# Optimization experiments

Hardware: AMD Instinct MI355X
Metric: run time of the kernel (lower is better)

Reference implementation:

```python
import jax, jax.numpy as jnp
import numpy as np
from jax import lax

B, N, CIN, H, W = 1, 6, 256, 32, 88
COUT = 80
IMG_H, IMG_W = 256, 704
XB = (-51.2, 51.2, 0.8); YB = (-51.2, 51.2, 0.8); ZB = (-5.0, 3.0, 0.8)
NX, NY, NZ = 128, 128, 10
EPS = 1e-5


def _voxel_coords(b0, b1, vs):
    n = int(round((b1 - b0) / vs))
    return jnp.linspace(b0 + 0.5 * vs, b1 - 0.5 * vs, n, dtype=jnp.float32)


def _make_points():
    xs = _voxel_coords(*XB); ys = _voxel_coords(*YB); zs = _voxel_coords(*ZB)
    gx, gy, gz = jnp.meshgrid(xs, ys, zs, indexing='ij')
    return jnp.stack([gx, gy, gz], -1).reshape(-1, 3)  # [M,3], M = NX*NY*NZ


def _conv(x, w, b=None, pad=1):
    y = lax.conv_general_dilated(x, w, (1, 1), [(pad, pad), (pad, pad)],
                                 dimension_numbers=('NCHW', 'OIHW', 'NCHW'))
    if b is not None:
        y = y + b[None, :, None, None]
    return y


def _bn(x, g, b, m, v):
    return (g[None, :, None, None] * (x - m[None, :, None, None])
            * lax.rsqrt(v[None, :, None, None] + EPS) + b[None, :, None, None])


def _bilinear(feat, gx, gy):
    # feat [C,Hf,Wf]; gx,gy [M] in [-1,1]; align_corners=True, zero padding
    C, Hf, Wf = feat.shape
    ix = (gx + 1.0) * 0.5 * (Wf - 1)
    iy = (gy + 1.0) * 0.5 * (Hf - 1)
    ix0 = jnp.floor(ix); iy0 = jnp.floor(iy)
    wx1 = ix - ix0; wy1 = iy - iy0

    def tap(iyf, ixf, wgt):
        valid = (ixf >= 0) & (ixf < Wf) & (iyf >= 0) & (iyf < Hf)
        ii = jnp.clip(ixf, 0, Wf - 1).astype(jnp.int32)
        jj = jnp.clip(iyf, 0, Hf - 1).astype(jnp.int32)
        return feat[:, jj, ii] * (wgt * valid)[None, :]

    return (tap(iy0, ix0, (1 - wy1) * (1 - wx1))
            + tap(iy0, ix0 + 1, (1 - wy1) * wx1)
            + tap(iy0 + 1, ix0, wy1 * (1 - wx1))
            + tap(iy0 + 1, ix0 + 1, wy1 * wx1))


def reference(img, lidar2image, w1, b1, g1, beta1, m1, v1,
              w2, b2, g2, beta2, m2, v2, w3, b3):
    # proj_net: conv3x3+BN+ReLU, conv3x3+BN+ReLU, conv1x1
    x = img.reshape(B * N, CIN, H, W)
    x = jax.nn.relu(_bn(_conv(x, w1, b1), g1, beta1, m1, v1))
    x = jax.nn.relu(_bn(_conv(x, w2, b2), g2, beta2, m2, v2))
    feat = _conv(x, w3, b3, pad=0)  # [B*N, COUT, H, W]

    pts = _make_points()  # [M,3]
    R = lidar2image[:, :, :3, :3].reshape(B * N, 3, 3)
    t = lidar2image[:, :, :3, 3].reshape(B * N, 3, 1)
    proj = jnp.einsum('kij,mj->kim', R, pts) + t  # [BN,3,M]
    dist = proj[:, 2]
    px = proj[:, 0] / dist
    py = proj[:, 1] / dist
    gx = px / IMG_W * 2.0 - 1.0
    gy = py / IMG_H * 2.0 - 1.0

    sampled = jax.vmap(_bilinear)(feat, gx, gy)  # [BN, COUT, M]
    on_img = (px < IMG_W) & (px > 0) & (py < IMG_H) & (py > 0) & (dist > 0.1)
    sampled = jnp.where(on_img[:, None, :], sampled, 0.0)

    vox = sampled.reshape(B, N, COUT, NX, NY, NZ)
    bev = jnp.max(vox, axis=1).mean(axis=-1)  # [B, COUT, NX, NY]
    return bev


def setup_inputs() -> dict:
    key = jax.random.key(0)
    ks = jax.random.split(key, 8)
    img = jax.random.normal(ks[0], (B, N, CIN, H, W), jnp.float32)

    # Plausible lidar->image matrices: 6 cameras in a ring, pinhole intrinsics.
    fx = fy = 280.0; cx = IMG_W / 2.0; cy = IMG_H / 2.0
    K = np.array([[fx, 0.0, cx], [0.0, fy, cy], [0.0, 0.0, 1.0]])
    mats = []
    for k in range(N):
        th = 2.0 * np.pi * k / N
        fwd = np.array([np.cos(th), np.sin(th), 0.0])
        rgt = np.array([np.sin(th), -np.cos(th), 0.0])
        dwn = np.array([0.0, 0.0, -1.0])
        Rm = np.stack([rgt, dwn, fwd], 0)
        c = np.array([0.5 * np.cos(th), 0.5 * np.sin(th), 1.5])
        M4 = np.eye(4)
        M4[:3, :3] = K @ Rm
        M4[:3, 3] = K @ (-Rm @ c)
        mats.append(M4)
    lidar2image = jnp.asarray(np.broadcast_to(np.stack(mats), (B, N, 4, 4)).copy(),
                              jnp.float32)

    def w(k, shape, s=0.02):
        return jax.random.normal(k, shape, jnp.float32) * s

    zc = lambda c: jnp.zeros((c,), jnp.float32)
    oc = lambda c: jnp.ones((c,), jnp.float32)
    return dict(
        img=img, lidar2image=lidar2image,
        w1=w(ks[1], (CIN, CIN, 3, 3)), b1=zc(CIN),
        g1=oc(CIN), beta1=zc(CIN), m1=zc(CIN), v1=oc(CIN),
        w2=w(ks[2], (CIN, CIN, 3, 3)), b2=zc(CIN),
        g2=oc(CIN), beta2=zc(CIN), m2=zc(CIN), v2=oc(CIN),
        w3=w(ks[3], (COUT, CIN, 1, 1)), b3=zc(COUT),
    )
```

## Files before the change

### kernel.cpp

```cpp
#include <hip/hip_runtime.h>
#include <math.h>

#define N_IMG 6
#define CIN   256
#define H_IN  32
#define W_IN  88
#define SP    2816
#define HH    34
#define WW    90
#define SPH   3060
#define COUTC 80
#define EPSBN 1e-5f

typedef _Float16 half8 __attribute__((ext_vector_type(8)));
typedef _Float16 half2v __attribute__((ext_vector_type(2)));
typedef float floatx4 __attribute__((ext_vector_type(4)));

#define AS1 __attribute__((address_space(1)))
#define AS3 __attribute__((address_space(3)))

__global__ __launch_bounds__(256) void zero_halo(_Float16* __restrict__ a,
                                                 _Float16* __restrict__ b) {
  const int im = blockIdx.x;
  const int tid = threadIdx.x;
  for (int s = tid; s < 244 * 32; s += 256) {
    const int pos = s >> 5;
    const int gr  = s & 31;
    int h, w;
    if (pos < 90)       { h = 0;  w = pos; }
    else if (pos < 180) { h = 33; w = pos - 90; }
    else { const int r = pos - 180; h = 1 + (r >> 1); w = (r & 1) * 89; }
    const size_t off = ((size_t)im * SPH + h * WW + w) * CIN + gr * 8;
    half8 z = {};
    *(half8*)(a + off) = z;
    *(half8*)(b + off) = z;
  }
}

__global__ __launch_bounds__(256) void prep_w33(const float* __restrict__ wa,
                                                const float* __restrict__ wb,
                                                _Float16* __restrict__ wTa,
                                                _Float16* __restrict__ wTb) {
  __shared__ float s[2304];
  const int oc = blockIdx.x;
  const int tid = threadIdx.x;
  const float* w = blockIdx.y ? wb : wa;
  _Float16* wT = blockIdx.y ? wTb : wTa;
  const float* wo = w + (size_t)oc * 2304;
  for (int i = tid; i < 2304; i += 256) s[i] = wo[i];
  __syncthreads();
  for (int i = tid; i < 2304; i += 256) {
    const int tap = i >> 8;
    const int ic  = i & 255;
    wT[((size_t)tap * 256 + oc) * 256 + ic] = (_Float16)s[ic * 9 + tap];
  }
}

__global__ __launch_bounds__(256) void prep_w11(const float* __restrict__ w,
                                                _Float16* __restrict__ wT) {
  int idx = blockIdx.x * 256 + threadIdx.x;
  if (idx >= CIN * COUTC) return;
  wT[idx] = (_Float16)w[idx];
}

__global__ __launch_bounds__(256) void nchw_to_nhwc(const float* __restrict__ img,
                                                    _Float16* __restrict__ x0) {
  __shared__ float t[64][65];
  const int sp0 = blockIdx.x * 64;
  const int ic0 = blockIdx.y * 64;
  const int im  = blockIdx.z;
  const int tx = threadIdx.x & 63;
  const int ty = threadIdx.x >> 6;
  for (int r = ty; r < 64; r += 4)
    t[r][tx] = img[((size_t)(im * CIN + ic0 + r)) * SP + sp0 + tx];
  __syncthreads();
  for (int r = ty; r < 64; r += 4) {
    const int sp = sp0 + r;
    const int h = sp / 88;
    const int w = sp - h * 88;
    x0[((size_t)im * SPH + h * WW + w + WW + 1) * CIN + ic0 + tx] = (_Float16)t[tx][r];
  }
}

__global__ __launch_bounds__(256) void conv3x3_mfma(
    const _Float16* __restrict__ x, const _Float16* __restrict__ wT,
    const float* __restrict__ bias, const float* __restrict__ gamma,
    const float* __restrict__ beta, const float* __restrict__ bnm,
    const float* __restrict__ bnv, _Float16* __restrict__ out,
    int OW, int OB, int imStride)
{
  __shared__ _Float16 As[128 * 64];
  __shared__ _Float16 Bs[128 * 64];

  const int tid  = threadIdx.x;
  const int wv   = tid >> 6;
  const int lane = tid & 63;
  const int m0   = blockIdx.x * 128;
  const int n0   = blockIdx.y * 128;
  const int im   = blockIdx.z;
  const _Float16* xim = x + (size_t)im * SPH * CIN;

  int srcA[4], srcB[4];
  #pragma unroll
  for (int i = 0; i < 4; ++i) {
    const int g = i * 256 + wv * 64 + lane;
    const int row = g >> 3;
    const int lg  = (g & 7) ^ (row & 7);
    const int m = m0 + row;
    const int h = m / 88;
    const int w = m - h * 88;
    srcA[i] = ((h + 1) * WW + (w + 1)) * CIN + lg * 8;
    srcB[i] = (n0 + row) * 256 + lg * 8;
  }

  const int fr = lane & 15;
  const int q  = lane >> 4;
  const int q4 = q * 4;
  const int mw = (wv & 1) * 64;
  const int nw = (wv >> 1) * 64;

  floatx4 acc[4][4];
  #pragma unroll
  for (int i = 0; i < 4; ++i)
    #pragma unroll
    for (int j = 0; j < 4; ++j) {
      acc[i][j][0] = 0.f; acc[i][j][1] = 0.f; acc[i][j][2] = 0.f; acc[i][j][3] = 0.f;
    }

  for (int tap = 0; tap < 9; ++tap) {
    const int dy = tap / 3 - 1;
    const int dx = tap - (tap / 3) * 3 - 1;
    const int aoff = (dy * WW + dx) * CIN;
    const size_t boff = (size_t)tap * 65536;

    for (int icc = 0; icc < 256; icc += 64) {
      #pragma unroll
      for (int i = 0; i < 4; ++i)
        __builtin_amdgcn_global_load_lds(
            (const AS1 void*)(xim + srcA[i] + aoff + icc),
            (AS3 void*)(&As[(i * 256 + wv * 64) * 8]), 16, 0, 0);
      #pragma unroll
      for (int i = 0; i < 4; ++i)
        __builtin_amdgcn_global_load_lds(
            (const AS1 void*)(wT + boff + srcB[i] + icc),
            (AS3 void*)(&Bs[(i * 256 + wv * 64) * 8]), 16, 0, 0);
      __syncthreads();

      #pragma unroll
      for (int ks = 0; ks < 2; ++ks) {
        half8 af[4], bf[4];
        #pragma unroll
        for (int i = 0; i < 4; ++i) {
          const int row = mw + i * 16 + fr;
          af[i] = *(const half8*)(&As[row * 64 + (((ks * 4 + q) ^ (row & 7)) * 8)]);
        }
        #pragma unroll
        for (int j = 0; j < 4; ++j) {
          const int row = nw + j * 16 + fr;
          bf[j] = *(const half8*)(&Bs[row * 64 + (((ks * 4 + q) ^ (row & 7)) * 8)]);
        }
        #pragma unroll
        for (int i = 0; i < 4; ++i)
          #pragma unroll
          for (int j = 0; j < 4; ++j)
            acc[i][j] = __builtin_amdgcn_mfma_f32_16x16x32_f16(af[i], bf[j], acc[i][j], 0, 0, 0);
      }
      __syncthreads();
    }
  }

  #pragma unroll
  for (int j = 0; j < 4; ++j) {
    const int oc = n0 + nw + j * 16 + fr;
    const float sc = gamma[oc] * rsqrtf(bnv[oc] + EPSBN);
    const float sh = (bias[oc] - bnm[oc]) * sc + beta[oc];
    #pragma unroll
    for (int i = 0; i < 4; ++i) {
      #pragma unroll
      for (int r = 0; r < 4; ++r) {
        const int m = m0 + mw + i * 16 + q4 + r;
        const int h = m / 88;
        const int w = m - h * 88;
        const float v = fmaxf(fmaf(acc[i][j][r], sc, sh), 0.f);
        out[((size_t)im * imStride + h * OW + w + OB) * CIN + oc] = (_Float16)v;
      }
    }
  }
}

__global__ __launch_bounds__(128) void conv1x1_mfma(
    const _Float16* __restrict__ x, const _Float16* __restrict__ wT,
    const float* __restrict__ bias, _Float16* __restrict__ feat)
{
  __shared__ _Float16 Bs[80 * 264];

  const int tid = threadIdx.x;
  const int m0  = blockIdx.x * 64;
  const int wv   = tid >> 6;
  const int lane = tid & 63;
  const int fr  = lane & 15;
  const int q8  = (lane >> 4) * 8;
  const int q4  = (lane >> 4) * 4;

  for (int g = tid; g < 2560; g += 128) {
    const int oc = g >> 5;
    const int kg8 = (g & 31) << 3;
    *(half8*)(&Bs[oc * 264 + kg8]) = *(const half8*)(wT + oc * 256 + kg8);
  }
  __syncthreads();

  floatx4 acc[2][5];
  #pragma unroll
  for (int i = 0; i < 2; ++i)
    #pragma unroll
    for (int j = 0; j < 5; ++j) {
      acc[i][j][0] = 0.f; acc[i][j][1] = 0.f; acc[i][j][2] = 0.f; acc[i][j][3] = 0.f;
    }

  const _Float16* xa = x + (size_t)(m0 + wv * 32 + fr) * 256 + q8;
  #pragma unroll
  for (int ks = 0; ks < 8; ++ks) {
    half8 af[2], bf[5];
    #pragma unroll
    for (int i = 0; i < 2; ++i)
      af[i] = *(const half8*)(xa + (size_t)i * 16 * 256 + ks * 32);
    #pragma unroll
    for (int j = 0; j < 5; ++j)
      bf[j] = *(const half8*)(&Bs[(j * 16 + fr) * 264 + ks * 32 + q8]);
    #pragma unroll
    for (int i = 0; i < 2; ++i)
      #pragma unroll
      for (int j = 0; j < 5; ++j)
        acc[i][j] = __builtin_amdgcn_mfma_f32_16x16x32_f16(af[i], bf[j], acc[i][j], 0, 0, 0);
  }

  #pragma unroll
  for (int j = 0; j < 5; ++j) {
    const int oc = j * 16 + fr;
    const float bb = bias[oc];
    #pragma unroll
    for (int i = 0; i < 2; ++i) {
      const int mbase = m0 + wv * 32 + i * 16 + q4;
      #pragma unroll
      for (int r = 0; r < 4; ++r)
        feat[(size_t)(mbase + r) * COUTC + oc] = (_Float16)(acc[i][j][r] + bb);
    }
  }
}

__global__ __launch_bounds__(320) void bev_sample(
    const _Float16* __restrict__ feat, const float* __restrict__ l2i,
    float* __restrict__ tmp)
{
  __shared__ int4   eo[480];
  __shared__ float4 ew[480];
  const int tid = threadIdx.x;
  const int cellBase = blockIdx.x * 8;

  for (int e = tid; e < 480; e += 320) {
    const int cell = e / 60;
    const int idx = e - cell * 60;
    const int n = idx / 10;
    const int z = idx - n * 10;
    const int cid = cellBase + cell;
    const int gix = cid >> 7;
    const int giy = cid & 127;
    const float X = (float)(-50.8 + (double)gix * (101.6 / 127.0));
    const float Y = (float)(-50.8 + (double)giy * (101.6 / 127.0));
    const float Z = (float)(-4.6 + (double)z * (7.2 / 9.0));
    const float* M = l2i + n * 16;
    const float pw = M[0] * X + M[1] * Y + M[2] * Z + M[3];
    const float ph = M[4] * X + M[5] * Y + M[6] * Z + M[7];
    const float d  = M[8] * X + M[9] * Y + M[10] * Z + M[11];
    const float px = pw / d;
    const float py = ph / d;
    const bool on_img = (px < 704.f) && (px > 0.f) && (py < 256.f) && (py > 0.f) && (d > 0.1f);
    const float gx = px / 704.f * 2.f - 1.f;
    const float gy = py / 256.f * 2.f - 1.f;
    const float ixf = (gx + 1.f) * 0.5f * 87.f;
    const float iyf = (gy + 1.f) * 0.5f * 31.f;
    const float ix0 = floorf(ixf);
    const float iy0 = floorf(iyf);
    const float wx1 = ixf - ix0;
    const float wy1 = iyf - iy0;
    const float ix1 = ix0 + 1.f, iy1 = iy0 + 1.f;
    float w00 = (1.f - wy1) * (1.f - wx1);
    float w01 = (1.f - wy1) * wx1;
    float w10 = wy1 * (1.f - wx1);
    float w11 = wy1 * wx1;
    const bool vx0 = (ix0 >= 0.f) && (ix0 < 88.f);
    const bool vx1 = (ix1 >= 0.f) && (ix1 < 88.f);
    const bool vy0 = (iy0 >= 0.f) && (iy0 < 32.f);
    const bool vy1 = (iy1 >= 0.f) && (iy1 < 32.f);
    if (!(on_img && vy0 && vx0)) w00 = 0.f;
    if (!(on_img && vy0 && vx1)) w01 = 0.f;
    if (!(on_img && vy1 && vx0)) w10 = 0.f;
    if (!(on_img && vy1 && vx1)) w11 = 0.f;
    const int i0 = (int)fminf(fmaxf(ix0, 0.f), 87.f);
    const int i1 = (int)fminf(fmaxf(ix1, 0.f), 87.f);
    const int j0 = (int)fminf(fmaxf(iy0, 0.f), 31.f);
    const int j1 = (int)fminf(fmaxf(iy1, 0.f), 31.f);
    const int base = n * SP;
    eo[e] = make_int4((base + j0 * 88 + i0) * COUTC,
                      (base + j0 * 88 + i1) * COUTC,
                      (base + j1 * 88 + i0) * COUTC,
                      (base + j1 * 88 + i1) * COUTC);
    ew[e] = make_float4(w00, w01, w10, w11);
  }
  __syncthreads();

  const int c2 = (tid % 40) * 2;
  const int cell = tid / 40;
  const int ebase = cell * 60;
  float a0 = 0.f, a1 = 0.f;
  for (int z = 0; z < 10; ++z) {
    float mx0 = -INFINITY, mx1 = -INFINITY;
    #pragma unroll
    for (int n = 0; n < 6; ++n) {
      const float4 w = ew[ebase + n * 10 + z];
      if (w.x + w.y + w.z + w.w > 0.f) {
        const int4 o = eo[ebase + n * 10 + z];
        const half2v p00 = *(const half2v*)(feat + o.x + c2);
        const half2v p01 = *(const half2v*)(feat + o.y + c2);
        const half2v p10 = *(const half2v*)(feat + o.z + c2);
        const half2v p11 = *(const half2v*)(feat + o.w + c2);
        float v0 = w.x * (float)p00[0];
        float v1 = w.x * (float)p00[1];
        v0 = fmaf(w.y, (float)p01[0], v0);  v1 = fmaf(w.y, (float)p01[1], v1);
        v0 = fmaf(w.z, (float)p10[0], v0);  v1 = fmaf(w.z, (float)p10[1], v1);
        v0 = fmaf(w.w, (float)p11[0], v0);  v1 = fmaf(w.w, (float)p11[1], v1);
        mx0 = fmaxf(mx0, v0);
        mx1 = fmaxf(mx1, v1);
      } else {
        mx0 = fmaxf(mx0, 0.f);
        mx1 = fmaxf(mx1, 0.f);
      }
    }
    a0 += mx0;
    a1 += mx1;
  }
  const int cid = cellBase + cell;
  float2 res = make_float2(a0 * 0.1f, a1 * 0.1f);
  *(float2*)(&tmp[(size_t)cid * COUTC + c2]) = res;
}

__global__ __launch_bounds__(256) void bev_transpose(const float* __restrict__ tmp,
                                                     float* __restrict__ out)
{
  __shared__ float tile[32][33];
  const int mBase = blockIdx.x * 32;
  const int cBase = blockIdx.y * 32;
  const int tx = threadIdx.x & 31;
  const int ty = threadIdx.x >> 5;
  for (int i = ty; i < 32; i += 8) {
    const int cc = cBase + tx;
    tile[i][tx] = (cc < COUTC) ? tmp[(size_t)(mBase + i) * COUTC + cc] : 0.f;
  }
  __syncthreads();
  for (int i = ty; i < 32; i += 8) {
    const int cc = cBase + i;
    if (cc < COUTC) out[(size_t)cc * 16384 + mBase + tx] = tile[tx][i];
  }
}

extern "C" void kernel_launch(void* const* d_in, const int* in_sizes, int n_in,
                              void* d_out, int out_size, void* d_ws, size_t ws_size,
                              hipStream_t stream)
{
  const float* img = (const float*)d_in[0];
  const float* l2i = (const float*)d_in[1];
  const float* w1  = (const float*)d_in[2];
  const float* b1  = (const float*)d_in[3];
  const float* g1  = (const float*)d_in[4];
  const float* be1 = (const float*)d_in[5];
  const float* m1  = (const float*)d_in[6];
  const float* v1  = (const float*)d_in[7];
  const float* w2  = (const float*)d_in[8];
  const float* b2  = (const float*)d_in[9];
  const float* g2  = (const float*)d_in[10];
  const float* be2 = (const float*)d_in[11];
  const float* m2  = (const float*)d_in[12];
  const float* v2  = (const float*)d_in[13];
  const float* w3  = (const float*)d_in[14];
  const float* b3  = (const float*)d_in[15];

  char* ws = (char*)d_ws;
  _Float16* wT1h = (_Float16*)ws;  ws += (size_t)9 * CIN * CIN * 2;
  _Float16* wT2h = (_Float16*)ws;  ws += (size_t)9 * CIN * CIN * 2;
  _Float16* wT3h = (_Float16*)ws;  ws += (size_t)CIN * COUTC * 2;
  _Float16* x0   = (_Float16*)ws;  ws += (size_t)N_IMG * SPH * CIN * 2;
  _Float16* x1h  = (_Float16*)ws;  ws += (size_t)N_IMG * SPH * CIN * 2;
  _Float16* x2h  = (_Float16*)ws;  ws += (size_t)N_IMG * SP * CIN * 2;
  _Float16* feat = (_Float16*)ws;  ws += (size_t)N_IMG * SP * COUTC * 2;
  float*    tmp  = (float*)ws;
  float*    outp = (float*)d_out;

  zero_halo<<<6, 256, 0, stream>>>(x0, x1h);
  prep_w33<<<dim3(256, 2), 256, 0, stream>>>(w1, w2, wT1h, wT2h);
  prep_w11<<<80, 256, 0, stream>>>(w3, wT3h);
  nchw_to_nhwc<<<dim3(44, 4, 6), 256, 0, stream>>>(img, x0);

  conv3x3_mfma<<<dim3(22, 2, 6), 256, 0, stream>>>(x0, wT1h, b1, g1, be1, m1, v1,
                                                   x1h, WW, WW + 1, SPH);
  conv3x3_mfma<<<dim3(22, 2, 6), 256, 0, stream>>>(x1h, wT2h, b2, g2, be2, m2, v2,
                                                   x2h, 88, 0, SP);
  conv1x1_mfma<<<264, 128, 0, stream>>>(x2h, wT3h, b3, feat);

  bev_sample<<<2048, 320, 0, stream>>>(feat, l2i, tmp);
  bev_transpose<<<dim3(512, 3), 256, 0, stream>>>(tmp, outp);
}
```

Baseline: 223.1 us.

## Double-buffer conv3x3 LDS tiles and merge halo-zero with 1x1 weight prep

The conv3x3 MFMA kernel now keeps two LDS buffers for the A and B tiles. It issues the global-to-LDS loads for the next K chunk before computing on the current one, using a single barrier per chunk instead of two, so memory latency can hide behind MFMA work. Separately, the zero_halo and prep_w11 kernels are merged into one launch to save a kernel launch. LDS use per block doubles to 64KB, which may cut occupancy. The async global_load_lds writes rely on the single barrier for ordering.

```diff
diff --git a/kernel.cpp b/kernel.cpp
--- a/kernel.cpp
+++ b/kernel.cpp
@@ -18,24 +18,6 @@
 
 #define AS1 __attribute__((address_space(1)))
 #define AS3 __attribute__((address_space(3)))
-
-__global__ __launch_bounds__(256) void zero_halo(_Float16* __restrict__ a,
-                                                 _Float16* __restrict__ b) {
-  const int im = blockIdx.x;
-  const int tid = threadIdx.x;
-  for (int s = tid; s < 244 * 32; s += 256) {
-    const int pos = s >> 5;
-    const int gr  = s & 31;
-    int h, w;
-    if (pos < 90)       { h = 0;  w = pos; }
-    else if (pos < 180) { h = 33; w = pos - 90; }
-    else { const int r = pos - 180; h = 1 + (r >> 1); w = (r & 1) * 89; }
-    const size_t off = ((size_t)im * SPH + h * WW + w) * CIN + gr * 8;
-    half8 z = {};
-    *(half8*)(a + off) = z;
-    *(half8*)(b + off) = z;
-  }
-}
 
 __global__ __launch_bounds__(256) void prep_w33(const float* __restrict__ wa,
                                                 const float* __restrict__ wb,
@@ -56,11 +38,30 @@
   }
 }
 
-__global__ __launch_bounds__(256) void prep_w11(const float* __restrict__ w,
-                                                _Float16* __restrict__ wT) {
-  int idx = blockIdx.x * 256 + threadIdx.x;
-  if (idx >= CIN * COUTC) return;
-  wT[idx] = (_Float16)w[idx];
+__global__ __launch_bounds__(256) void prep_misc(const float* __restrict__ w3,
+                                                 _Float16* __restrict__ wT3,
+                                                 _Float16* __restrict__ a,
+                                                 _Float16* __restrict__ b) {
+  const int bx = blockIdx.x;
+  const int tid = threadIdx.x;
+  if (bx < 80) {
+    const int idx = bx * 256 + tid;
+    wT3[idx] = (_Float16)w3[idx];
+  } else {
+    const int im = bx - 80;
+    for (int s = tid; s < 244 * 32; s += 256) {
+      const int pos = s >> 5;
+      const int gr  = s & 31;
+      int h, w;
+      if (pos < 90)       { h = 0;  w = pos; }
+      else if (pos < 180) { h = 33; w = pos - 90; }
+      else { const int r = pos - 180; h = 1 + (r >> 1); w = (r & 1) * 89; }
+      const size_t off = ((size_t)im * SPH + h * WW + w) * CIN + gr * 8;
+      half8 z = {};
+      *(half8*)(a + off) = z;
+      *(half8*)(b + off) = z;
+    }
+  }
 }
 
 __global__ __launch_bounds__(256) void nchw_to_nhwc(const float* __restrict__ img,
@@ -89,8 +90,8 @@
     const float* __restrict__ bnv, _Float16* __restrict__ out,
     int OW, int OB, int imStride)
 {
-  __shared__ _Float16 As[128 * 64];
-  __shared__ _Float16 Bs[128 * 64];
+  __shared__ _Float16 As[2][128 * 64];
+  __shared__ _Float16 Bs[2][128 * 64];
 
   const int tid  = threadIdx.x;
   const int wv   = tid >> 6;
@@ -127,45 +128,61 @@
       acc[i][j][0] = 0.f; acc[i][j][1] = 0.f; acc[i][j][2] = 0.f; acc[i][j][3] = 0.f;
     }
 
-  for (int tap = 0; tap < 9; ++tap) {
-    const int dy = tap / 3 - 1;
-    const int dx = tap - (tap / 3) * 3 - 1;
-    const int aoff = (dy * WW + dx) * CIN;
-    const size_t boff = (size_t)tap * 65536;
-
-    for (int icc = 0; icc < 256; icc += 64) {
+  {
+    const int aoff0 = (-1 * WW - 1) * CIN;
+    #pragma unroll
+    for (int i = 0; i < 4; ++i)
+      __builtin_amdgcn_global_load_lds(
+          (const AS1 void*)(xim + srcA[i] + aoff0),
+          (AS3 void*)(&As[0][(i * 256 + wv * 64) * 8]), 16, 0, 0);
+    #pragma unroll
+    for (int i = 0; i < 4; ++i)
+      __builtin_amdgcn_global_load_lds(
+          (const AS1 void*)(wT + srcB[i]),
+          (AS3 void*)(&Bs[0][(i * 256 + wv * 64) * 8]), 16, 0, 0);
+  }
+
+  for (int c = 0; c < 36; ++c) {
+    __syncthreads();
+    if (c < 35) {
+      const int cn   = c + 1;
+      const int tapn = cn >> 2;
+      const int iccn = (cn & 3) << 6;
+      const int dyn  = tapn / 3 - 1;
+      const int dxn  = tapn - (tapn / 3) * 3 - 1;
+      const int aoffn = (dyn * WW + dxn) * CIN + iccn;
+      const size_t boffn = (size_t)tapn * 65536 + iccn;
+      const int nb = cn & 1;
       #pragma unroll
       for (int i = 0; i < 4; ++i)
         __builtin_amdgcn_global_load_lds(
-            (const AS1 void*)(xim + srcA[i] + aoff + icc),
-            (AS3 void*)(&As[(i * 256 + wv * 64) * 8]), 16, 0, 0);
+            (const AS1 void*)(xim + srcA[i] + aoffn),
+            (AS3 void*)(&As[nb][(i * 256 + wv * 64) * 8]), 16, 0, 0);
       #pragma unroll
       for (int i = 0; i < 4; ++i)
         __builtin_amdgcn_global_load_lds(
-            (const AS1 void*)(wT + boff + srcB[i] + icc),
-            (AS3 void*)(&Bs[(i * 256 + wv * 64) * 8]), 16, 0, 0);
-      __syncthreads();
-
-      #pragma unroll
-      for (int ks = 0; ks < 2; ++ks) {
-        half8 af[4], bf[4];
+            (const AS1 void*)(wT + boffn + srcB[i]),
+            (AS3 void*)(&Bs[nb][(i * 256 + wv * 64) * 8]), 16, 0, 0);
+    }
+    const int cb = c & 1;
+    #pragma unroll
+    for (int ks = 0; ks < 2; ++ks) {
+      half8 af[4], bf[4];
+      #pragma unroll
+      for (int i = 0; i < 4; ++i) {
+        const int row = mw + i * 16 + fr;
+        af[i] = *(const half8*)(&As[cb][row * 64 + (((ks * 4 + q) ^ (row & 7)) * 8)]);
+      }
+      #pragma unroll
+      for (int j = 0; j < 4; ++j) {
+        const int row = nw + j * 16 + fr;
+        bf[j] = *(const half8*)(&Bs[cb][row * 64 + (((ks * 4 + q) ^ (row & 7)) * 8)]);
+      }
+      #pragma unroll
+      for (int i = 0; i < 4; ++i)
         #pragma unroll
-        for (int i = 0; i < 4; ++i) {
-          const int row = mw + i * 16 + fr;
-          af[i] = *(const half8*)(&As[row * 64 + (((ks * 4 + q) ^ (row & 7)) * 8)]);
-        }
-        #pragma unroll
-        for (int j = 0; j < 4; ++j) {
-          const int row = nw + j * 16 + fr;
-          bf[j] = *(const half8*)(&Bs[row * 64 + (((ks * 4 + q) ^ (row & 7)) * 8)]);
-        }
-        #pragma unroll
-        for (int i = 0; i < 4; ++i)
-          #pragma unroll
-          for (int j = 0; j < 4; ++j)
-            acc[i][j] = __builtin_amdgcn_mfma_f32_16x16x32_f16(af[i], bf[j], acc[i][j], 0, 0, 0);
-      }
-      __syncthreads();
+        for (int j = 0; j < 4; ++j)
+          acc[i][j] = __builtin_amdgcn_mfma_f32_16x16x32_f16(af[i], bf[j], acc[i][j], 0, 0, 0);
     }
   }
 
@@ -395,9 +412,8 @@
   float*    tmp  = (float*)ws;
   float*    outp = (float*)d_out;
 
-  zero_halo<<<6, 256, 0, stream>>>(x0, x1h);
+  prep_misc<<<86, 256, 0, stream>>>(w3, wT3h, x0, x1h);
   prep_w33<<<dim3(256, 2), 256, 0, stream>>>(w1, w2, wT1h, wT2h);
-  prep_w11<<<80, 256, 0, stream>>>(w3, wT3h);
   nchw_to_nhwc<<<dim3(44, 4, 6), 256, 0, stream>>>(img, x0);
 
   conv3x3_mfma<<<dim3(22, 2, 6), 256, 0, stream>>>(x0, wT1h, b1, g1, be1, m1, v1,
```

Result: slower. 249.1 us (+11.6%).

## Shrink conv3x3 N-tile to 64 with grid-stride tiles; merge small prep kernels

Applied to the files above, without the earlier changes.

The 3x3 conv kernel moves from 128x128 output tiles (264 blocks) to 128x64 tiles (528 tiles) processed by a 512-block grid-stride loop. Tiles are ordered so that the four N-tiles sharing one A tile sit next to each other, which should help L2 reuse. The intent is to fill all CUs of the MI355X more evenly, since 264 blocks leave many CUs idle. The cost is more redundant A loads per output and a lower MFMA-to-load ratio. The halo zeroing and 1x1 weight conversion are merged into one launch to save a kernel launch.

```diff
diff --git a/kernel.cpp b/kernel.cpp
--- a/kernel.cpp
+++ b/kernel.cpp
@@ -18,24 +18,6 @@
 
 #define AS1 __attribute__((address_space(1)))
 #define AS3 __attribute__((address_space(3)))
-
-__global__ __launch_bounds__(256) void zero_halo(_Float16* __restrict__ a,
-                                                 _Float16* __restrict__ b) {
-  const int im = blockIdx.x;
-  const int tid = threadIdx.x;
-  for (int s = tid; s < 244 * 32; s += 256) {
-    const int pos = s >> 5;
-    const int gr  = s & 31;
-    int h, w;
-    if (pos < 90)       { h = 0;  w = pos; }
-    else if (pos < 180) { h = 33; w = pos - 90; }
-    else { const int r = pos - 180; h = 1 + (r >> 1); w = (r & 1) * 89; }
-    const size_t off = ((size_t)im * SPH + h * WW + w) * CIN + gr * 8;
-    half8 z = {};
-    *(half8*)(a + off) = z;
-    *(half8*)(b + off) = z;
-  }
-}
 
 __global__ __launch_bounds__(256) void prep_w33(const float* __restrict__ wa,
                                                 const float* __restrict__ wb,
@@ -56,11 +38,30 @@
   }
 }
 
-__global__ __launch_bounds__(256) void prep_w11(const float* __restrict__ w,
-                                                _Float16* __restrict__ wT) {
-  int idx = blockIdx.x * 256 + threadIdx.x;
-  if (idx >= CIN * COUTC) return;
-  wT[idx] = (_Float16)w[idx];
+__global__ __launch_bounds__(256) void prep_misc(const float* __restrict__ w3,
+                                                 _Float16* __restrict__ wT3,
+                                                 _Float16* __restrict__ a,
+                                                 _Float16* __restrict__ b) {
+  const int bx = blockIdx.x;
+  const int tid = threadIdx.x;
+  if (bx < 80) {
+    const int idx = bx * 256 + tid;
+    wT3[idx] = (_Float16)w3[idx];
+  } else {
+    const int im = bx - 80;
+    for (int s = tid; s < 244 * 32; s += 256) {
+      const int pos = s >> 5;
+      const int gr  = s & 31;
+      int h, w;
+      if (pos < 90)       { h = 0;  w = pos; }
+      else if (pos < 180) { h = 33; w = pos - 90; }
+      else { const int r = pos - 180; h = 1 + (r >> 1); w = (r & 1) * 89; }
+      const size_t off = ((size_t)im * SPH + h * WW + w) * CIN + gr * 8;
+      half8 z = {};
+      *(half8*)(a + off) = z;
+      *(half8*)(b + off) = z;
+    }
+  }
 }
 
 __global__ __launch_bounds__(256) void nchw_to_nhwc(const float* __restrict__ img,
@@ -90,99 +91,107 @@
     int OW, int OB, int imStride)
 {
   __shared__ _Float16 As[128 * 64];
-  __shared__ _Float16 Bs[128 * 64];
+  __shared__ _Float16 Bs[64 * 64];
 
   const int tid  = threadIdx.x;
   const int wv   = tid >> 6;
   const int lane = tid & 63;
-  const int m0   = blockIdx.x * 128;
-  const int n0   = blockIdx.y * 128;
-  const int im   = blockIdx.z;
-  const _Float16* xim = x + (size_t)im * SPH * CIN;
-
-  int srcA[4], srcB[4];
-  #pragma unroll
-  for (int i = 0; i < 4; ++i) {
-    const int g = i * 256 + wv * 64 + lane;
-    const int row = g >> 3;
-    const int lg  = (g & 7) ^ (row & 7);
-    const int m = m0 + row;
-    const int h = m / 88;
-    const int w = m - h * 88;
-    srcA[i] = ((h + 1) * WW + (w + 1)) * CIN + lg * 8;
-    srcB[i] = (n0 + row) * 256 + lg * 8;
-  }
-
-  const int fr = lane & 15;
-  const int q  = lane >> 4;
-  const int q4 = q * 4;
-  const int mw = (wv & 1) * 64;
-  const int nw = (wv >> 1) * 64;
-
-  floatx4 acc[4][4];
-  #pragma unroll
-  for (int i = 0; i < 4; ++i)
-    #pragma unroll
-    for (int j = 0; j < 4; ++j) {
-      acc[i][j][0] = 0.f; acc[i][j][1] = 0.f; acc[i][j][2] = 0.f; acc[i][j][3] = 0.f;
-    }
-
-  for (int tap = 0; tap < 9; ++tap) {
-    const int dy = tap / 3 - 1;
-    const int dx = tap - (tap / 3) * 3 - 1;
-    const int aoff = (dy * WW + dx) * CIN;
-    const size_t boff = (size_t)tap * 65536;
-
-    for (int icc = 0; icc < 256; icc += 64) {
+  const int fr   = lane & 15;
+  const int q    = lane >> 4;
+  const int q4   = q * 4;
+  const int mw   = (wv & 1) * 64;
+  const int nw   = (wv >> 1) * 32;
+
+  for (int t = blockIdx.x; t < 528; t += 512) {
+    const int n0   = (t & 3) << 6;
+    const int mt   = t >> 2;
+    const int im   = mt / 22;
+    const int m0sp = (mt - im * 22) * 128;
+    const _Float16* xim = x + (size_t)im * SPH * CIN;
+
+    int srcA[4], srcB[2];
+    #pragma unroll
+    for (int i = 0; i < 4; ++i) {
+      const int g = i * 256 + wv * 64 + lane;
+      const int row = g >> 3;
+      const int lg  = (g & 7) ^ (row & 7);
+      const int m = m0sp + row;
+      const int h = m / 88;
+      const int w = m - h * 88;
+      srcA[i] = ((h + 1) * WW + (w + 1)) * CIN + lg * 8;
+    }
+    #pragma unroll
+    for (int i = 0; i < 2; ++i) {
+      const int g = i * 256 + wv * 64 + lane;
+      const int row = g >> 3;
+      const int lg  = (g & 7) ^ (row & 7);
+      srcB[i] = (n0 + row) * 256 + lg * 8;
+    }
+
+    floatx4 acc[4][2];
+    #pragma unroll
+    for (int i = 0; i < 4; ++i)
+      #pragma unroll
+      for (int j = 0; j < 2; ++j) {
+        acc[i][j][0] = 0.f; acc[i][j][1] = 0.f; acc[i][j][2] = 0.f; acc[i][j][3] = 0.f;
+      }
+
+    for (int c = 0; c < 36; ++c) {
+      const int tap = c >> 2;
+      const int icc = (c & 3) << 6;
+      const int dy  = tap / 3 - 1;
+      const int dx  = tap - (tap / 3) * 3 - 1;
+      const int aoff = (dy * WW + dx) * CIN + icc;
+      const size_t boff = (size_t)tap * 65536 + icc;
       #pragma unroll
       for (int i = 0; i < 4; ++i)
         __builtin_amdgcn_global_load_lds(
-            (const AS1 void*)(xim + srcA[i] + aoff + icc),
+            (const AS1 void*)(xim + srcA[i] + aoff),
             (AS3 void*)(&As[(i * 256 + wv * 64) * 8]), 16, 0, 0);
       #pragma unroll
-      for (int i = 0; i < 4; ++i)
+      for (int i = 0; i < 2; ++i)
         __builtin_amdgcn_global_load_lds(
-            (const AS1 void*)(wT + boff + srcB[i] + icc),
+            (const AS1 void*)(wT + boff + srcB[i]),
             (AS3 void*)(&Bs[(i * 256 + wv * 64) * 8]), 16, 0, 0);
       __syncthreads();
 
       #pragma unroll
       for (int ks = 0; ks < 2; ++ks) {
-        half8 af[4], bf[4];
+        half8 af[4], bf[2];
         #pragma unroll
         for (int i = 0; i < 4; ++i) {
           const int row = mw + i * 16 + fr;
           af[i] = *(const half8*)(&As[row * 64 + (((ks * 4 + q) ^ (row & 7)) * 8)]);
         }
         #pragma unroll
-        for (int j = 0; j < 4; ++j) {
+        for (int j = 0; j < 2; ++j) {
           const int row = nw + j * 16 + fr;
           bf[j] = *(const half8*)(&Bs[row * 64 + (((ks * 4 + q) ^ (row & 7)) * 8)]);
         }
         #pragma unroll
         for (int i = 0; i < 4; ++i)
           #pragma unroll
-          for (int j = 0; j < 4; ++j)
+          for (int j = 0; j < 2; ++j)
             acc[i][j] = __builtin_amdgcn_mfma_f32_16x16x32_f16(af[i], bf[j], acc[i][j], 0, 0, 0);
       }
       __syncthreads();
     }
-  }
-
-  #pragma unroll
-  for (int j = 0; j < 4; ++j) {
-    const int oc = n0 + nw + j * 16 + fr;
-    const float sc = gamma[oc] * rsqrtf(bnv[oc] + EPSBN);
-    const float sh = (bias[oc] - bnm[oc]) * sc + beta[oc];
-    #pragma unroll
-    for (int i = 0; i < 4; ++i) {
-      #pragma unroll
-      for (int r = 0; r < 4; ++r) {
-        const int m = m0 + mw + i * 16 + q4 + r;
-        const int h = m / 88;
-        const int w = m - h * 88;
-        const float v = fmaxf(fmaf(acc[i][j][r], sc, sh), 0.f);
-        out[((size_t)im * imStride + h * OW + w + OB) * CIN + oc] = (_Float16)v;
+
+    #pragma unroll
+    for (int j = 0; j < 2; ++j) {
+      const int oc = n0 + nw + j * 16 + fr;
+      const float sc = gamma[oc] * rsqrtf(bnv[oc] + EPSBN);
+      const float sh = (bias[oc] - bnm[oc]) * sc + beta[oc];
+      #pragma unroll
+      for (int i = 0; i < 4; ++i) {
+        #pragma unroll
+        for (int r = 0; r < 4; ++r) {
+          const int m = m0sp + mw + i * 16 + q4 + r;
+          const int h = m / 88;
+          const int w = m - h * 88;
+          const float v = fmaxf(fmaf(acc[i][j][r], sc, sh), 0.f);
+          out[((size_t)im * imStride + h * OW + w + OB) * CIN + oc] = (_Float16)v;
+        }
       }
     }
   }
@@ -395,15 +404,14 @@
   float*    tmp  = (float*)ws;
   float*    outp = (float*)d_out;
 
-  zero_halo<<<6, 256, 0, stream>>>(x0, x1h);
+  prep_misc<<<86, 256, 0, stream>>>(w3, wT3h, x0, x1h);
   prep_w33<<<dim3(256, 2), 256, 0, stream>>>(w1, w2, wT1h, wT2h);
-  prep_w11<<<80, 256, 0, stream>>>(w3, wT3h);
   nchw_to_nhwc<<<dim3(44, 4, 6), 256, 0, stream>>>(img, x0);
 
-  conv3x3_mfma<<<dim3(22, 2, 6), 256, 0, stream>>>(x0, wT1h, b1, g1, be1, m1, v1,
-                                                   x1h, WW, WW + 1, SPH);
-  conv3x3_mfma<<<dim3(22, 2, 6), 256, 0, stream>>>(x1h, wT2h, b2, g2, be2, m2, v2,
-                                                   x2h, 88, 0, SP);
+  conv3x3_mfma<<<512, 256, 0, stream>>>(x0, wT1h, b1, g1, be1, m1, v1,
+                                        x1h, WW, WW + 1, SPH);
+  conv3x3_mfma<<<512, 256, 0, stream>>>(x1h, wT2h, b2, g2, be2, m2, v2,
+                                        x2h, 88, 0, SP);
   conv1x1_mfma<<<264, 128, 0, stream>>>(x2h, wT3h, b3, feat);
 
   bev_sample<<<2048, 320, 0, stream>>>(feat, l2i, tmp);
```

Result: slower. 264.8 us (+18.7%).

## Stage full-K weight tile in LDS per tap and load activations directly from global

Applied to the files above, without the earlier changes.

The 3x3 conv kernel now stages the whole 128x256 weight slice for each tap in LDS (64 KB) and reads the activation fragments straight from global memory into registers, with no A staging. This cuts the barriers from eight per tap to two. The grid is flattened so the two N-halves of the same M tile are adjacent blocks and can share activations in L2. Separately, the halo-zeroing and 1x1 weight-prep kernels are merged into one launch. In exchange, the larger LDS footprint lowers occupancy and the uncoalesced global A loads can stall the MFMA pipeline.

```diff
diff --git a/kernel.cpp b/kernel.cpp
--- a/kernel.cpp
+++ b/kernel.cpp
@@ -18,24 +18,6 @@
 
 #define AS1 __attribute__((address_space(1)))
 #define AS3 __attribute__((address_space(3)))
-
-__global__ __launch_bounds__(256) void zero_halo(_Float16* __restrict__ a,
-                                                 _Float16* __restrict__ b) {
-  const int im = blockIdx.x;
-  const int tid = threadIdx.x;
-  for (int s = tid; s < 244 * 32; s += 256) {
-    const int pos = s >> 5;
-    const int gr  = s & 31;
-    int h, w;
-    if (pos < 90)       { h = 0;  w = pos; }
-    else if (pos < 180) { h = 33; w = pos - 90; }
-    else { const int r = pos - 180; h = 1 + (r >> 1); w = (r & 1) * 89; }
-    const size_t off = ((size_t)im * SPH + h * WW + w) * CIN + gr * 8;
-    half8 z = {};
-    *(half8*)(a + off) = z;
-    *(half8*)(b + off) = z;
-  }
-}
 
 __global__ __launch_bounds__(256) void prep_w33(const float* __restrict__ wa,
                                                 const float* __restrict__ wb,
@@ -56,11 +38,30 @@
   }
 }
 
-__global__ __launch_bounds__(256) void prep_w11(const float* __restrict__ w,
-                                                _Float16* __restrict__ wT) {
-  int idx = blockIdx.x * 256 + threadIdx.x;
-  if (idx >= CIN * COUTC) return;
-  wT[idx] = (_Float16)w[idx];
+__global__ __launch_bounds__(256) void prep_misc(const float* __restrict__ w3,
+                                                 _Float16* __restrict__ wT3,
+                                                 _Float16* __restrict__ a,
+                                                 _Float16* __restrict__ b) {
+  const int bx = blockIdx.x;
+  const int tid = threadIdx.x;
+  if (bx < 80) {
+    const int idx = bx * 256 + tid;
+    wT3[idx] = (_Float16)w3[idx];
+  } else {
+    const int im = bx - 80;
+    for (int s = tid; s < 244 * 32; s += 256) {
+      const int pos = s >> 5;
+      const int gr  = s & 31;
+      int h, w;
+      if (pos < 90)       { h = 0;  w = pos; }
+      else if (pos < 180) { h = 33; w = pos - 90; }
+      else { const int r = pos - 180; h = 1 + (r >> 1); w = (r & 1) * 89; }
+      const size_t off = ((size_t)im * SPH + h * WW + w) * CIN + gr * 8;
+      half8 z = {};
+      *(half8*)(a + off) = z;
+      *(half8*)(b + off) = z;
+    }
+  }
 }
 
 __global__ __launch_bounds__(256) void nchw_to_nhwc(const float* __restrict__ img,
@@ -89,35 +90,50 @@
     const float* __restrict__ bnv, _Float16* __restrict__ out,
     int OW, int OB, int imStride)
 {
-  __shared__ _Float16 As[128 * 64];
-  __shared__ _Float16 Bs[128 * 64];
+  __shared__ _Float16 Bs[128 * 256];
 
   const int tid  = threadIdx.x;
   const int wv   = tid >> 6;
   const int lane = tid & 63;
-  const int m0   = blockIdx.x * 128;
-  const int n0   = blockIdx.y * 128;
-  const int im   = blockIdx.z;
+  const int bx   = blockIdx.x;
+  const int n0   = (bx & 1) << 7;
+  const int mt   = bx >> 1;
+  const int im   = mt / 22;
+  const int m0sp = (mt - im * 22) * 128;
   const _Float16* xim = x + (size_t)im * SPH * CIN;
-
-  int srcA[4], srcB[4];
-  #pragma unroll
-  for (int i = 0; i < 4; ++i) {
-    const int g = i * 256 + wv * 64 + lane;
-    const int row = g >> 3;
-    const int lg  = (g & 7) ^ (row & 7);
-    const int m = m0 + row;
-    const int h = m / 88;
-    const int w = m - h * 88;
-    srcA[i] = ((h + 1) * WW + (w + 1)) * CIN + lg * 8;
-    srcB[i] = (n0 + row) * 256 + lg * 8;
-  }
 
   const int fr = lane & 15;
   const int q  = lane >> 4;
+  const int q8 = q * 8;
   const int q4 = q * 4;
   const int mw = (wv & 1) * 64;
   const int nw = (wv >> 1) * 64;
+
+  int spBase[4];
+  #pragma unroll
+  for (int i = 0; i < 4; ++i) {
+    const int m = m0sp + mw + i * 16 + fr;
+    const int h = m / 88;
+    const int w = m - h * 88;
+    spBase[i] = ((h + 1) * WW + (w + 1)) * CIN + q8;
+  }
+
+  int srcB[16];
+  #pragma unroll
+  for (int t = 0; t < 16; ++t) {
+    const int g   = (t * 4 + wv) * 64 + lane;
+    const int row = g >> 5;
+    const int col = g & 31;
+    srcB[t] = (n0 + row) * 256 + ((col ^ (row & 7)) * 8);
+  }
+
+  int bRow[4], bKey[4];
+  #pragma unroll
+  for (int j = 0; j < 4; ++j) {
+    const int r = nw + j * 16 + fr;
+    bRow[j] = r * 256;
+    bKey[j] = r & 7;
+  }
 
   floatx4 acc[4][4];
   #pragma unroll
@@ -133,31 +149,28 @@
     const int aoff = (dy * WW + dx) * CIN;
     const size_t boff = (size_t)tap * 65536;
 
+    __syncthreads();
+    #pragma unroll
+    for (int t = 0; t < 16; ++t)
+      __builtin_amdgcn_global_load_lds(
+          (const AS1 void*)(wT + boff + srcB[t]),
+          (AS3 void*)(&Bs[(t * 4 + wv) * 512]), 16, 0, 0);
+    __syncthreads();
+
+    #pragma unroll
     for (int icc = 0; icc < 256; icc += 64) {
-      #pragma unroll
-      for (int i = 0; i < 4; ++i)
-        __builtin_amdgcn_global_load_lds(
-            (const AS1 void*)(xim + srcA[i] + aoff + icc),
-            (AS3 void*)(&As[(i * 256 + wv * 64) * 8]), 16, 0, 0);
-      #pragma unroll
-      for (int i = 0; i < 4; ++i)
-        __builtin_amdgcn_global_load_lds(
-            (const AS1 void*)(wT + boff + srcB[i] + icc),
-            (AS3 void*)(&Bs[(i * 256 + wv * 64) * 8]), 16, 0, 0);
-      __syncthreads();
-
+      const int gbase = icc >> 3;
       #pragma unroll
       for (int ks = 0; ks < 2; ++ks) {
         half8 af[4], bf[4];
+        const int koff = aoff + icc + ks * 32;
         #pragma unroll
-        for (int i = 0; i < 4; ++i) {
-          const int row = mw + i * 16 + fr;
-          af[i] = *(const half8*)(&As[row * 64 + (((ks * 4 + q) ^ (row & 7)) * 8)]);
-        }
+        for (int i = 0; i < 4; ++i)
+          af[i] = *(const half8*)(xim + spBase[i] + koff);
         #pragma unroll
         for (int j = 0; j < 4; ++j) {
-          const int row = nw + j * 16 + fr;
-          bf[j] = *(const half8*)(&Bs[row * 64 + (((ks * 4 + q) ^ (row & 7)) * 8)]);
+          const int g = gbase + ks * 4 + q;
+          bf[j] = *(const half8*)(&Bs[bRow[j] + ((g ^ bKey[j]) * 8)]);
         }
         #pragma unroll
         for (int i = 0; i < 4; ++i)
@@ -165,7 +178,6 @@
           for (int j = 0; j < 4; ++j)
             acc[i][j] = __builtin_amdgcn_mfma_f32_16x16x32_f16(af[i], bf[j], acc[i][j], 0, 0, 0);
       }
-      __syncthreads();
     }
   }
 
@@ -178,7 +190,7 @@
     for (int i = 0; i < 4; ++i) {
       #pragma unroll
       for (int r = 0; r < 4; ++r) {
-        const int m = m0 + mw + i * 16 + q4 + r;
+        const int m = m0sp + mw + i * 16 + q4 + r;
         const int h = m / 88;
         const int w = m - h * 88;
         const float v = fmaxf(fmaf(acc[i][j][r], sc, sh), 0.f);
@@ -395,15 +407,14 @@
   float*    tmp  = (float*)ws;
   float*    outp = (float*)d_out;
 
-  zero_halo<<<6, 256, 0, stream>>>(x0, x1h);
+  prep_misc<<<86, 256, 0, stream>>>(w3, wT3h, x0, x1h);
   prep_w33<<<dim3(256, 2), 256, 0, stream>>>(w1, w2, wT1h, wT2h);
-  prep_w11<<<80, 256, 0, stream>>>(w3, wT3h);
   nchw_to_nhwc<<<dim3(44, 4, 6), 256, 0, stream>>>(img, x0);
 
-  conv3x3_mfma<<<dim3(22, 2, 6), 256, 0, stream>>>(x0, wT1h, b1, g1, be1, m1, v1,
-                                                   x1h, WW, WW + 1, SPH);
-  conv3x3_mfma<<<dim3(22, 2, 6), 256, 0, stream>>>(x1h, wT2h, b2, g2, be2, m2, v2,
-                                                   x2h, 88, 0, SP);
+  conv3x3_mfma<<<264, 256, 0, stream>>>(x0, wT1h, b1, g1, be1, m1, v1,
+                                        x1h, WW, WW + 1, SPH);
+  conv3x3_mfma<<<264, 256, 0, stream>>>(x1h, wT2h, b2, g2, be2, m2, v2,
+                                        x2h, 88, 0, SP);
   conv1x1_mfma<<<264, 128, 0, stream>>>(x2h, wT3h, b3, feat);
 
   bev_sample<<<2048, 320, 0, stream>>>(feat, l2i, tmp);
```

New measurement: 298.4 us. 33.7% more time.
